# Kernel optimization log

Hardware: AMD Instinct MI355X
Metric: run time of the kernel (lower is better)

The kernel has to match this reference:

```python
import jax, jax.numpy as jnp
import numpy as np

N_USERS = 1_000_000
N_ITEMS = 100_000
D = 64        # embedding dim
B = 16384     # batch of (user, pos-set, neg-item) triples
S = 20        # size of positive item set


def setup_inputs() -> dict:
    key = jax.random.key(0)
    k1, k2, k3, k4, k5, k6 = jax.random.split(key, 6)
    # original init: (rand - 0.5) * 0.01  -> uniform in (-0.005, 0.005)
    U = (jax.random.uniform(k1, (N_USERS, D), dtype=jnp.float32) - 0.5) * 0.01
    V = (jax.random.uniform(k2, (N_ITEMS, D), dtype=jnp.float32) - 0.5) * 0.01
    bi = jax.random.normal(k3, (N_ITEMS,), dtype=jnp.float32) * 0.01
    user_id = jax.random.randint(k4, (B,), 0, N_USERS, dtype=jnp.int64)
    pos_item_id = jax.random.randint(k5, (B, S), 0, N_ITEMS, dtype=jnp.int64)
    neg_item_id = jax.random.randint(k6, (B,), 0, N_ITEMS, dtype=jnp.int64)
    return {"U": U, "V": V, "bi": bi, "user_id": user_id,
            "pos_item_id": pos_item_id, "neg_item_id": neg_item_id}


def reference(U, V, bi, user_id, pos_item_id, neg_item_id):
    # Fused gather + row-wise dot (replaces diag(matmul) anti-pattern).
    u = U[user_id]                                   # [B, D]
    vp = V[pos_item_id]                              # [B, S, D]
    # caculate_score_pos: mean over the item set of (u . v_i + b_i)
    pos = (jnp.einsum('bd,bsd->bs', u, vp) + bi[pos_item_id]).mean(axis=1)  # [B]
    # caculate_score_neg: u . v_j + b_j
    vn = V[neg_item_id]                              # [B, D]
    neg = jnp.einsum('bd,bd->b', u, vn) + bi[neg_item_id]                   # [B]
    return jnp.stack([pos, neg])                     # [2, B]
```

## Files before the change

### kernel.cpp

```cpp
#include <hip/hip_runtime.h>
#include <hip/hip_bf16.h>


#define DIM 64
#define NPOS 20

__global__ __launch_bounds__(256) void cofiset_kernel(
    const float* __restrict__ U,
    const float* __restrict__ V,
    const float* __restrict__ bi,
    const int*   __restrict__ user_id,
    const int*   __restrict__ pos_item_id,
    const int*   __restrict__ neg_item_id,
    float* __restrict__ out,
    int B)
{
    const int gwave = (int)((blockIdx.x * blockDim.x + threadIdx.x) >> 6);
    const int lane  = (int)(threadIdx.x & 63);
    const int r     = lane >> 4;
    const int q     = lane & 15;
    const int row   = gwave * 4 + r;
    if (row >= B) return;

    const int uid  = user_id[row];
    const int nidx = neg_item_id[row];
    const int pidx  = pos_item_id[row * NPOS + q];
    const int pidx2 = (q < 4) ? pos_item_id[row * NPOS + 16 + q] : 0;

    const float4 u4 = *(const float4*)&U[(size_t)uid * DIM + q * 4];

    float acc = bi[pidx] + ((q < 4) ? bi[pidx2] : 0.0f);
    const float nb = bi[nidx];

    const float4 vn = *(const float4*)&V[(size_t)nidx * DIM + q * 4];
    float accn = u4.x * vn.x + u4.y * vn.y + u4.z * vn.z + u4.w * vn.w;

    const int grp = lane & 48;
    #pragma unroll
    for (int s = 0; s < NPOS; ++s) {
        const int idx = (s < 16) ? __shfl(pidx,  grp + s)
                                 : __shfl(pidx2, grp + (s - 16));
        const float4 v4 = *(const float4*)&V[(size_t)idx * DIM + q * 4];
        acc = fmaf(u4.x, v4.x, acc);
        acc = fmaf(u4.y, v4.y, acc);
        acc = fmaf(u4.z, v4.z, acc);
        acc = fmaf(u4.w, v4.w, acc);
    }

    #pragma unroll
    for (int off = 8; off >= 1; off >>= 1) {
        acc  += __shfl_xor(acc,  off);
        accn += __shfl_xor(accn, off);
    }

    if (q == 0) {
        out[row]     = acc * (1.0f / (float)NPOS);
        out[B + row] = accn + nb;
    }
}

extern "C" void kernel_launch(void* const* d_in, const int* in_sizes, int n_in,
                              void* d_out, int out_size, void* d_ws, size_t ws_size,
                              hipStream_t stream) {
    const float* U   = (const float*)d_in[0];
    const float* V   = (const float*)d_in[1];
    const float* bi  = (const float*)d_in[2];
    const int* user_id     = (const int*)d_in[3];
    const int* pos_item_id = (const int*)d_in[4];
    const int* neg_item_id = (const int*)d_in[5];
    float* out = (float*)d_out;

    const int B = in_sizes[3];
    const int rows_per_block = 4 * 4;
    const int grid = (B + rows_per_block - 1) / rows_per_block;

    cofiset_kernel<<<grid, 256, 0, stream>>>(U, V, bi, user_id, pos_item_id,
                                             neg_item_id, out, B);
}
```

Measured before the change: 18.58 us.

## Assign one row per wave, splitting positive items across lane groups

Each wave now processes a single row instead of four, with each 16-lane group gathering 5 of the 20 positive items, followed by a full-wave reduction. The grid is enlarged accordingly. This shortens the serial chain of dependent gathers per thread and increases memory-level parallelism. In exchange, U rows are loaded redundantly by four groups, more waves are launched, and the negative-item dot product runs on only one group.

```diff
diff --git a/kernel.cpp b/kernel.cpp
--- a/kernel.cpp
+++ b/kernel.cpp
@@ -15,31 +15,28 @@
     float* __restrict__ out,
     int B)
 {
-    const int gwave = (int)((blockIdx.x * blockDim.x + threadIdx.x) >> 6);
-    const int lane  = (int)(threadIdx.x & 63);
-    const int r     = lane >> 4;
-    const int q     = lane & 15;
-    const int row   = gwave * 4 + r;
+    const int row  = (int)((blockIdx.x * blockDim.x + threadIdx.x) >> 6);
+    const int lane = (int)(threadIdx.x & 63);
+    const int r    = lane >> 4;
+    const int q    = lane & 15;
     if (row >= B) return;
 
     const int uid  = user_id[row];
     const int nidx = neg_item_id[row];
-    const int pidx  = pos_item_id[row * NPOS + q];
-    const int pidx2 = (q < 4) ? pos_item_id[row * NPOS + 16 + q] : 0;
+    int pidx = 0;
+    float pb = 0.0f;
+    if (q < 5) {
+        pidx = pos_item_id[row * NPOS + r * 5 + q];
+        pb   = bi[pidx];
+    }
 
     const float4 u4 = *(const float4*)&U[(size_t)uid * DIM + q * 4];
 
-    float acc = bi[pidx] + ((q < 4) ? bi[pidx2] : 0.0f);
-    const float nb = bi[nidx];
-
-    const float4 vn = *(const float4*)&V[(size_t)nidx * DIM + q * 4];
-    float accn = u4.x * vn.x + u4.y * vn.y + u4.z * vn.z + u4.w * vn.w;
-
-    const int grp = lane & 48;
+    const int grp = r << 4;
+    float acc = pb;
     #pragma unroll
-    for (int s = 0; s < NPOS; ++s) {
-        const int idx = (s < 16) ? __shfl(pidx,  grp + s)
-                                 : __shfl(pidx2, grp + (s - 16));
+    for (int j = 0; j < 5; ++j) {
+        const int idx = __shfl(pidx, grp + j);
         const float4 v4 = *(const float4*)&V[(size_t)idx * DIM + q * 4];
         acc = fmaf(u4.x, v4.x, acc);
         acc = fmaf(u4.y, v4.y, acc);
@@ -47,15 +44,24 @@
         acc = fmaf(u4.w, v4.w, acc);
     }
 
+    float accn = 0.0f;
+    if (r == 0) {
+        const float4 vn = *(const float4*)&V[(size_t)nidx * DIM + q * 4];
+        accn = u4.x * vn.x + u4.y * vn.y + u4.z * vn.z + u4.w * vn.w;
+    }
+
+    #pragma unroll
+    for (int off = 32; off >= 1; off >>= 1) {
+        acc += __shfl_xor(acc, off);
+    }
     #pragma unroll
     for (int off = 8; off >= 1; off >>= 1) {
-        acc  += __shfl_xor(acc,  off);
         accn += __shfl_xor(accn, off);
     }
 
-    if (q == 0) {
+    if (lane == 0) {
         out[row]     = acc * (1.0f / (float)NPOS);
-        out[B + row] = accn + nb;
+        out[B + row] = accn + bi[nidx];
     }
 }
 
@@ -71,7 +77,7 @@
     float* out = (float*)d_out;
 
     const int B = in_sizes[3];
-    const int rows_per_block = 4 * 4;
+    const int rows_per_block = 4;
     const int grid = (B + rows_per_block - 1) / rows_per_block;
 
     cofiset_kernel<<<grid, 256, 0, stream>>>(U, V, bi, user_id, pos_item_id,
```

After: 19.29 us. +3.8%, slower.
